# Kernel tuning notes

Measured on AMD Instinct MI355X. Metric: run time of the kernel, lower is better.

The kernel has to match this reference:

```python
import jax, jax.numpy as jnp
import numpy as np

BEFORE_F = 12   # before_block_frames
AFTER_F = 6     # after_block_frames
FD = BEFORE_F // AFTER_F   # frame_duration = 2
K = 49          # cluster_num
L_TOK = 50      # num_tokens = 1 cls + before_cluster_num(49)
WIDTH = 768
B = 64
EPS_LN = 1e-5


def _layer_norm(x, w, b):
    mu = jnp.mean(x, axis=-1, keepdims=True)
    var = jnp.mean((x - mu) ** 2, axis=-1, keepdims=True)
    return (x - mu) / jnp.sqrt(var + EPS_LN) * w + b


def _cdist(a, b):
    # a: [N, L, D], b: [N, K, D] -> euclidean distances [N, L, K]
    d2 = (jnp.sum(a * a, -1)[:, :, None] + jnp.sum(b * b, -1)[:, None, :]
          - 2.0 * jnp.einsum('nld,nkd->nlk', a, b))
    return jnp.sqrt(jnp.maximum(d2, 0.0))


def setup_inputs() -> dict:
    key = jax.random.key(0)
    ks = jax.random.split(key, 4)
    d_in = FD * (L_TOK - 1)   # 98
    d_h = 4 * d_in            # 392
    d_mid = FD * K            # 98
    std = 0.01
    return {
        "x": jax.random.normal(ks[0], (L_TOK, B * BEFORE_F, WIDTH), jnp.float32),
        "fc1_w": jax.random.normal(ks[1], (d_in, d_h), jnp.float32) * std,
        "fc1_b": jnp.zeros((d_h,), jnp.float32),
        "ln1_w": jnp.ones((d_h,), jnp.float32),
        "ln1_b": jnp.zeros((d_h,), jnp.float32),
        "fc2_w": jax.random.normal(ks[2], (d_h, d_mid), jnp.float32) * std,
        "fc2_b": jnp.zeros((d_mid,), jnp.float32),
        "ln2_w": jnp.ones((d_mid,), jnp.float32),
        "ln2_b": jnp.zeros((d_mid,), jnp.float32),
        "fc3_w": jax.random.normal(ks[3], (d_mid, K), jnp.float32) * std,
        "fc3_b": jnp.zeros((K,), jnp.float32),
        "ln3_w": jnp.ones((K,), jnp.float32),
        "ln3_b": jnp.zeros((K,), jnp.float32),
    }


def reference(x, fc1_w, fc1_b, ln1_w, ln1_b, fc2_w, fc2_b, ln2_w, ln2_b,
              fc3_w, fc3_b, ln3_w, ln3_b):
    num_tokens, Bt, width = x.shape
    Bsz = Bt // BEFORE_F
    N = Bsz * AFTER_F
    xt = jnp.transpose(x, (1, 0, 2))                        # [Bt, L, D]

    # class token: mean over each frame_duration group -> [B*after, 1, D]
    cls = xt[:, 0, :].reshape(Bsz, AFTER_F, FD, width).mean(axis=2)
    class_embed = cls.reshape(N, 1, width)

    # patch tokens; torch.cat of splits along dim 0 gives (after, B) ordering
    res = xt[:, 1:, :].reshape(Bsz, AFTER_F, FD, num_tokens - 1, width)
    data = jnp.transpose(res, (1, 0, 2, 3, 4)).reshape(N, FD * (num_tokens - 1), width)
    d_data = jax.lax.stop_gradient(data)

    # token MLP over the token axis: [N, D, FD*(L-1)] -> [N, D, K]
    z = jnp.transpose(d_data, (0, 2, 1))
    z = _layer_norm(z @ fc1_w + fc1_b, ln1_w, ln1_b)
    z = _layer_norm(z @ fc2_w + fc2_b, ln2_w, ln2_b)
    z = _layer_norm(z @ fc3_w + fc3_b, ln3_w, ln3_b)
    centroids = jnp.transpose(z, (0, 2, 1))                 # [N, K, D]

    # wcss cluster loss (training path)
    dm = _cdist(d_data, centroids)                          # [N, L', K]
    cluster_loss = jnp.sum(jnp.min(dm, axis=-1), axis=-1).mean()

    # medoid selection: shift so every distance is negative, then masked min
    dm_s = dm - jnp.max(dm) - 1.0
    cd = jnp.min(dm_s, axis=-1)                             # [N, L']
    assign = jnp.argmin(dm_s, axis=-1)                      # [N, L']
    mask = assign[:, None, :] == jnp.arange(K)[None, :, None]   # [N, K, L']
    vals = jnp.where(mask, cd[:, None, :], 0.0)
    medoids = jnp.sort(jnp.argmin(vals, axis=-1), axis=1)   # [N, K]

    new_data = jnp.take_along_axis(data, medoids[:, :, None], axis=1)  # [N, K, D]
    # reorder (after, B) -> (B, after)
    sampled = jnp.transpose(new_data.reshape(AFTER_F, Bsz, K, width),
                            (1, 0, 2, 3)).reshape(N, K, width)
    out = jnp.concatenate([class_embed, sampled], axis=1)   # [N, K+1, D]
    out = jnp.transpose(out, (1, 0, 2))                     # [K+1, B*after, D]
    return out, cluster_loss
```

## Files before the change

### kernel.cpp

```cpp
#include <hip/hip_runtime.h>
#include <cstddef>

#define WIDTH 768
#define NTOK 98
#define DH 392
#define KCL 49
#define NGRP 384

typedef unsigned short ushort_t;
typedef unsigned int uint_t;
typedef __attribute__((ext_vector_type(4))) float f32x4;
typedef __attribute__((ext_vector_type(8))) short bf16x8;

static __device__ __forceinline__ ushort_t f2bf(float f) {
    union { float f; uint_t u; } v; v.f = f;
    uint_t u = v.u;
    uint_t r = (u + 0x7FFFu + ((u >> 16) & 1u)) >> 16;
    return (ushort_t)r;
}
static __device__ __forceinline__ uint_t pack2(float a, float b) {
    return (uint_t)f2bf(a) | ((uint_t)f2bf(b) << 16);
}

__global__ __launch_bounds__(256) void k_prep(
    const float* __restrict__ w1, const float* __restrict__ b1,
    const float* __restrict__ g1, const float* __restrict__ be1,
    const float* __restrict__ w2, const float* __restrict__ b2,
    const float* __restrict__ g2, const float* __restrict__ be2,
    const float* __restrict__ w3, const float* __restrict__ b3,
    ushort_t* __restrict__ w1T, ushort_t* __restrict__ w2T,
    ushort_t* __restrict__ w3T, float* __restrict__ bias2t)
{
    __shared__ float sb3[64];
    const int tid = threadIdx.x;
    if (blockIdx.x == 0) {
        if (tid < 98) {
            float s = b2[tid];
            for (int j = 0; j < DH; j++) s += be1[j] * w2[j * NTOK + tid];
            bias2t[tid] = s;
        }
        if (tid >= 128 && tid < 177) {
            int c = tid - 128;
            float s = b3[c];
            for (int j = 0; j < NTOK; j++) s += be2[j] * w3[j * KCL + c];
            sb3[c] = s;
        }
    }
    __syncthreads();
    if (blockIdx.x == 0 && tid < 64)
        w3T[tid * 128 + 98] = (tid < KCL) ? f2bf(sb3[tid]) : 0;

    for (int i = blockIdx.x * 256 + tid; i < 400 * 128; i += 1024) {
        int j = i >> 7, k = i & 127;
        float v = 0.f;
        if (j < DH) {
            if (k < NTOK) v = w1[k * DH + j];
            else if (k == NTOK) v = b1[j];
        }
        w1T[i] = f2bf(v);
    }
    for (int i = blockIdx.x * 256 + tid; i < 112 * 416; i += 1024) {
        int o = i / 416, k = i - o * 416;
        float v = 0.f;
        if (o < NTOK && k < DH) v = g1[k] * w2[k * NTOK + o];
        w2T[i] = f2bf(v);
    }
    for (int i = blockIdx.x * 256 + tid; i < 64 * 128; i += 1024) {
        int c = i >> 7, k = i & 127;
        if (k == NTOK) continue;
        float v = 0.f;
        if (c < KCL && k < NTOK) v = g2[k] * w3[k * KCL + c];
        w3T[i] = f2bf(v);
    }
}

__global__ __launch_bounds__(256, 2) void k_mlp(
    const float* __restrict__ x,
    const ushort_t* __restrict__ w1T, const ushort_t* __restrict__ w2T,
    const ushort_t* __restrict__ w3T, const float* __restrict__ bias2t,
    const float* __restrict__ g3, const float* __restrict__ be3,
    float* __restrict__ cent)
{
    __shared__ alignas(16) char smem[50176];

    const int tid = threadIdx.x;
    const int wv = tid >> 6;
    const int l = tid & 63;
    const int g = l >> 4;
    const int c16 = l & 15;

    const int n = blockIdx.x / 12;
    const int d0 = (blockIdx.x % 12) * 64;
    const int a = n >> 6, b = n & 63;
    const int bt0 = b * 12 + a * 2;

    {
        const int m = tid & 63;
        for (int oct = (tid >> 6); oct < 13; oct += 4) {
            ushort_t vals[8];
            #pragma unroll
            for (int e = 0; e < 8; e++) {
                int t = oct * 8 + e;
                float v;
                if (t < NTOK) {
                    int f = (t >= KCL), lt = t - f * KCL;
                    v = x[((size_t)(1 + lt) * WIDTH + bt0 + f) * WIDTH + d0 + m];
                } else v = (t == NTOK) ? 1.0f : 0.0f;
                vals[e] = f2bf(v);
            }
            uint4 u;
            u.x = (uint_t)vals[0] | ((uint_t)vals[1] << 16);
            u.y = (uint_t)vals[2] | ((uint_t)vals[3] << 16);
            u.z = (uint_t)vals[4] | ((uint_t)vals[5] << 16);
            u.w = (uint_t)vals[6] | ((uint_t)vals[7] << 16);
            *(uint4*)(smem + m * 256 + ((oct * 16) ^ ((m & 15) << 4))) = u;
        }
    }
    __syncthreads();

    bf16x8 bv[4];
    {
        const int mrow = wv * 16 + c16;
        #pragma unroll
        for (int ks = 0; ks < 4; ks++) {
            int oct = ks * 4 + g; if (oct > 12) oct = 12;
            bv[ks] = *(const bf16x8*)(smem + mrow * 256 + ((oct * 16) ^ ((mrow & 15) << 4)));
        }
    }
    __syncthreads();

    char* hbase = smem + wv * 12544 + c16 * 784;
    char* h2row = smem + wv * 12544 + c16 * 256;

    f32x4 acc1[25];
    #pragma unroll
    for (int T = 0; T < 25; T++) acc1[T] = (f32x4){0.f, 0.f, 0.f, 0.f};
    #pragma unroll
    for (int ks = 0; ks < 4; ks++) {
        #pragma unroll
        for (int T = 0; T < 25; T++) {
            const bf16x8 av = *(const bf16x8*)(w1T + (T * 16 + c16) * 128 + (ks * 4 + g) * 8);
            acc1[T] = __builtin_amdgcn_mfma_f32_16x16x32_bf16(av, bv[ks], acc1[T], 0, 0, 0);
        }
    }

    {
        float S = 0.f, Q = 0.f;
        #pragma unroll
        for (int T = 0; T < 25; T++) {
            f32x4 v = acc1[T];
            S += v.x + v.y + v.z + v.w;
            Q += v.x * v.x + v.y * v.y + v.z * v.z + v.w * v.w;
        }
        S += __shfl_xor(S, 16); Q += __shfl_xor(Q, 16);
        S += __shfl_xor(S, 32); Q += __shfl_xor(Q, 32);
        float mu = S * (1.f / DH);
        float var = Q * (1.f / DH) - mu * mu;
        float rstd = rsqrtf(fmaxf(var, 0.f) + 1e-5f);
        #pragma unroll
        for (int T = 0; T < 25; T++) {
            if (T == 24 && g >= 2) continue;
            f32x4 v = acc1[T];
            uint2 u;
            u.x = pack2((v.x - mu) * rstd, (v.y - mu) * rstd);
            u.y = pack2((v.z - mu) * rstd, (v.w - mu) * rstd);
            *(uint2*)(hbase + (T * 16 + g * 4) * 2) = u;
        }
    }

    f32x4 acc2[7];
    #pragma unroll
    for (int T = 0; T < 7; T++) acc2[T] = (f32x4){0.f, 0.f, 0.f, 0.f};
    #pragma unroll
    for (int ks = 0; ks < 13; ks++) {
        int oct = ks * 4 + g; if (oct > 48) oct = 48;
        const bf16x8 bvv = *(const bf16x8*)(hbase + oct * 16);
        #pragma unroll
        for (int T = 0; T < 7; T++) {
            const bf16x8 av = *(const bf16x8*)(w2T + (T * 16 + c16) * 416 + (ks * 4 + g) * 8);
            acc2[T] = __builtin_amdgcn_mfma_f32_16x16x32_bf16(av, bvv, acc2[T], 0, 0, 0);
        }
    }

    {
        #pragma unroll
        for (int T = 0; T < 7; T++) {
            int o0 = T * 16 + g * 4;
            #pragma unroll
            for (int r = 0; r < 4; r++) {
                int o = o0 + r;
                if (o < NTOK) acc2[T][r] += bias2t[o];
            }
        }
        float S = 0.f, Q = 0.f;
        #pragma unroll
        for (int T = 0; T < 7; T++) {
            f32x4 v = acc2[T];
            S += v.x + v.y + v.z + v.w;
            Q += v.x * v.x + v.y * v.y + v.z * v.z + v.w * v.w;
        }
        S += __shfl_xor(S, 16); Q += __shfl_xor(Q, 16);
        S += __shfl_xor(S, 32); Q += __shfl_xor(Q, 32);
        float mu = S * (1.f / NTOK);
        float var = Q * (1.f / NTOK) - mu * mu;
        float rstd = rsqrtf(fmaxf(var, 0.f) + 1e-5f);
        const int swz = (c16 & 7) << 4;
        #pragma unroll
        for (int T = 0; T < 7; T++) {
            f32x4 v = acc2[T];
            uint2 u;
            if (T < 6) {
                u.x = pack2((v.x - mu) * rstd, (v.y - mu) * rstd);
                u.y = pack2((v.z - mu) * rstd, (v.w - mu) * rstd);
            } else if (g == 0) {
                u.x = pack2((v.x - mu) * rstd, (v.y - mu) * rstd);
                u.y = pack2(1.0f, 0.0f);
            } else {
                u.x = 0u; u.y = 0u;
            }
            *(uint2*)(h2row + (((T * 16 + g * 4) * 2) ^ swz)) = u;
        }
        uint2 z; z.x = 0u; z.y = 0u;
        *(uint2*)(h2row + (((112 + g * 4) * 2) ^ swz)) = z;
    }

    f32x4 acc3[4];
    #pragma unroll
    for (int T = 0; T < 4; T++) acc3[T] = (f32x4){0.f, 0.f, 0.f, 0.f};
    {
        const int swz = (c16 & 7) << 4;
        #pragma unroll
        for (int ks = 0; ks < 4; ks++) {
            int oct = ks * 4 + g;
            const bf16x8 bvv = *(const bf16x8*)(h2row + ((oct * 16) ^ swz));
            #pragma unroll
            for (int T = 0; T < 4; T++) {
                const bf16x8 av = *(const bf16x8*)(w3T + (T * 16 + c16) * 128 + (ks * 4 + g) * 8);
                acc3[T] = __builtin_amdgcn_mfma_f32_16x16x32_bf16(av, bvv, acc3[T], 0, 0, 0);
            }
        }
    }

    {
        float S = 0.f, Q = 0.f;
        #pragma unroll
        for (int T = 0; T < 4; T++) {
            f32x4 v = acc3[T];
            S += v.x + v.y + v.z + v.w;
            Q += v.x * v.x + v.y * v.y + v.z * v.z + v.w * v.w;
        }
        S += __shfl_xor(S, 16); Q += __shfl_xor(Q, 16);
        S += __shfl_xor(S, 32); Q += __shfl_xor(Q, 32);
        float mu = S * (1.f / KCL);
        float var = Q * (1.f / KCL) - mu * mu;
        float rstd = rsqrtf(fmaxf(var, 0.f) + 1e-5f);
        const size_t cbase = (size_t)n * KCL * WIDTH + d0 + wv * 16 + c16;
        #pragma unroll
        for (int T = 0; T < 4; T++) {
            int c0 = T * 16 + g * 4;
            #pragma unroll
            for (int r = 0; r < 4; r++) {
                int c = c0 + r;
                if (c < KCL) {
                    float val = (acc3[T][r] - mu) * rstd * g3[c] + be3[c];
                    cent[cbase + (size_t)c * WIDTH] = val;
                }
            }
        }
    }
}

__global__ __launch_bounds__(256) void k_dist(
    const float* __restrict__ x, const float* __restrict__ cent,
    float* __restrict__ mind, int* __restrict__ assignp)
{
    int wid = blockIdx.x * 4 + (threadIdx.x >> 6);
    int lane = threadIdx.x & 63;
    int n = wid / 25, g = wid - n * 25;
    int t0 = g * 4;
    int a = n >> 6, b = n & 63;
    int bt0 = b * 12 + a * 2;

    float d[4][12];
    #pragma unroll
    for (int tt = 0; tt < 4; tt++) {
        int t = t0 + tt;
        bool valid = t < NTOK;
        int te = valid ? t : 0;
        int f = te / KCL, l = te - f * KCL;
        const float* src = x + ((size_t)(1 + l) * WIDTH + bt0 + f) * WIDTH + lane;
        #pragma unroll
        for (int i = 0; i < 12; i++) d[tt][i] = valid ? src[i * 64] : 0.f;
    }
    float nd[4];
    #pragma unroll
    for (int tt = 0; tt < 4; tt++) {
        float s = 0.f;
        #pragma unroll
        for (int i = 0; i < 12; i++) s = fmaf(d[tt][i], d[tt][i], s);
        #pragma unroll
        for (int o = 32; o > 0; o >>= 1) s += __shfl_xor(s, o);
        nd[tt] = s;
    }

    float minv[4] = {1e30f, 1e30f, 1e30f, 1e30f};
    int mini[4] = {0, 0, 0, 0};
    for (int k = 0; k < KCL; k++) {
        const float* cr = cent + ((size_t)n * KCL + k) * WIDTH + lane;
        float c[12];
        #pragma unroll
        for (int i = 0; i < 12; i++) c[i] = cr[i * 64];
        float cn = 0.f;
        #pragma unroll
        for (int i = 0; i < 12; i++) cn = fmaf(c[i], c[i], cn);
        float dot[4] = {0.f, 0.f, 0.f, 0.f};
        #pragma unroll
        for (int tt = 0; tt < 4; tt++)
            #pragma unroll
            for (int i = 0; i < 12; i++) dot[tt] = fmaf(d[tt][i], c[i], dot[tt]);
        #pragma unroll
        for (int o = 32; o > 0; o >>= 1) {
            cn += __shfl_xor(cn, o);
            #pragma unroll
            for (int tt = 0; tt < 4; tt++) dot[tt] += __shfl_xor(dot[tt], o);
        }
        #pragma unroll
        for (int tt = 0; tt < 4; tt++) {
            float dist = sqrtf(fmaxf(nd[tt] + cn - 2.f * dot[tt], 0.f));
            if (dist < minv[tt]) { minv[tt] = dist; mini[tt] = k; }
        }
    }
    if (lane == 0) {
        int nt = NTOK - t0; if (nt > 4) nt = 4;
        for (int tt = 0; tt < nt; tt++) {
            mind[n * NTOK + t0 + tt] = minv[tt];
            assignp[n * NTOK + t0 + tt] = mini[tt];
        }
    }
}

__global__ __launch_bounds__(256) void k_medoid(
    const float* __restrict__ x, const float* __restrict__ mind,
    const int* __restrict__ assignp, float* __restrict__ out)
{
    __shared__ float smind[NTOK];
    __shared__ int sassign[NTOK];
    __shared__ int med[KCL], sorted[KCL];

    int n = blockIdx.x, tid = threadIdx.x;
    int a = n >> 6, b = n & 63;
    int np = b * 6 + a;
    int bt0 = b * 12 + a * 2;

    if (tid < NTOK) { smind[tid] = mind[n * NTOK + tid]; sassign[tid] = assignp[n * NTOK + tid]; }
    __syncthreads();

    if (tid < KCL) {
        float best = 1e30f; int bi = 0;
        for (int t = 0; t < NTOK; t++)
            if (sassign[t] == tid && smind[t] < best) { best = smind[t]; bi = t; }
        med[tid] = bi;
    }
    __syncthreads();
    if (tid < KCL) {
        int mk = med[tid], rank = 0;
        for (int j = 0; j < KCL; j++) {
            int mj = med[j];
            rank += (mj < mk) || (mj == mk && j < tid);
        }
        sorted[rank] = mk;
    }
    __syncthreads();

    for (int dd = tid; dd < WIDTH; dd += 256)
        out[(size_t)np * WIDTH + dd] =
            0.5f * (x[(size_t)bt0 * WIDTH + dd] + x[(size_t)(bt0 + 1) * WIDTH + dd]);

    for (int k = 0; k < KCL; k++) {
        int m = sorted[k];
        int f = m / KCL, l = m - f * KCL;
        const float* src = x + ((size_t)(1 + l) * WIDTH + bt0 + f) * WIDTH;
        float* dst = out + ((size_t)(1 + k) * NGRP + np) * WIDTH;
        for (int dd = tid; dd < WIDTH; dd += 256) dst[dd] = src[dd];
    }
}

__global__ __launch_bounds__(256) void k_loss(const float* __restrict__ mind,
                                              float* __restrict__ out_loss)
{
    __shared__ float red[256];
    float s = 0.f;
    for (int i = threadIdx.x; i < NGRP * NTOK; i += 256) s += mind[i];
    red[threadIdx.x] = s;
    __syncthreads();
    for (int o = 128; o > 0; o >>= 1) {
        if (threadIdx.x < o) red[threadIdx.x] += red[threadIdx.x + o];
        __syncthreads();
    }
    if (threadIdx.x == 0) out_loss[0] = red[0] * (1.f / NGRP);
}

extern "C" void kernel_launch(void* const* d_in, const int* in_sizes, int n_in,
                              void* d_out, int out_size, void* d_ws, size_t ws_size,
                              hipStream_t stream)
{
    const float* x   = (const float*)d_in[0];
    const float* w1  = (const float*)d_in[1];
    const float* b1  = (const float*)d_in[2];
    const float* g1  = (const float*)d_in[3];
    const float* be1 = (const float*)d_in[4];
    const float* w2  = (const float*)d_in[5];
    const float* b2  = (const float*)d_in[6];
    const float* g2  = (const float*)d_in[7];
    const float* be2 = (const float*)d_in[8];
    const float* w3  = (const float*)d_in[9];
    const float* b3  = (const float*)d_in[10];
    const float* g3  = (const float*)d_in[11];
    const float* be3 = (const float*)d_in[12];
    float* out = (float*)d_out;

    float* cent = (float*)d_ws;
    float* mind = cent + (size_t)NGRP * KCL * WIDTH;
    int* assignp = (int*)(mind + NGRP * NTOK);
    ushort_t* w1T = (ushort_t*)(assignp + NGRP * NTOK);
    ushort_t* w2T = w1T + 400 * 128;
    ushort_t* w3T = w2T + 112 * 416;
    float* bias2t = (float*)(w3T + 64 * 128);

    k_prep<<<4, 256, 0, stream>>>(w1, b1, g1, be1, w2, b2, g2, be2, w3, b3,
                                  w1T, w2T, w3T, bias2t);
    k_mlp<<<NGRP * 12, 256, 0, stream>>>(x, w1T, w2T, w3T, bias2t, g3, be3, cent);
    k_dist<<<(NGRP * 25) / 4, 256, 0, stream>>>(x, cent, mind, assignp);
    k_medoid<<<NGRP, 256, 0, stream>>>(x, mind, assignp, out);
    k_loss<<<1, 256, 0, stream>>>(mind, out + (out_size - 1));
}
```

Baseline: 859.8 us.

## Defer LayerNorm normalization past next GEMM via rowsum correction, cut register pressure

The first and second LayerNorms are no longer applied before the following GEMM. Raw activations are stored and multiplied, and the normalization is folded in afterwards as rstd*(acc - mu*rowsum(W)) + bias, using row sums and biases precomputed in k_prep. The layer-1 GEMM now runs in chunks of five tiles instead of holding 25 accumulators at once, and the launch bound rises to 3 waves per SIMD to allow higher occupancy. The cost is extra numerical error, because unnormalized values are rounded to bf16 and a mean term is subtracted after accumulation.

```diff
diff --git a/kernel.cpp b/kernel.cpp
--- a/kernel.cpp
+++ b/kernel.cpp
@@ -29,26 +29,41 @@
     const float* __restrict__ g2, const float* __restrict__ be2,
     const float* __restrict__ w3, const float* __restrict__ b3,
     ushort_t* __restrict__ w1T, ushort_t* __restrict__ w2T,
-    ushort_t* __restrict__ w3T, float* __restrict__ bias2t)
-{
-    __shared__ float sb3[64];
+    ushort_t* __restrict__ w3T, float* __restrict__ bias2t,
+    float* __restrict__ rowsum2, float* __restrict__ rowsum3,
+    float* __restrict__ bias3t)
+{
     const int tid = threadIdx.x;
     if (blockIdx.x == 0) {
-        if (tid < 98) {
-            float s = b2[tid];
-            for (int j = 0; j < DH; j++) s += be1[j] * w2[j * NTOK + tid];
-            bias2t[tid] = s;
-        }
-        if (tid >= 128 && tid < 177) {
+        if (tid < 112) {
+            int o = tid;
+            float sb = 0.f, sr = 0.f;
+            if (o < NTOK) {
+                for (int j = 0; j < DH; j++) {
+                    float w = w2[j * NTOK + o];
+                    sb += be1[j] * w;
+                    sr += g1[j] * w;
+                }
+                sb += b2[o];
+            }
+            bias2t[o] = sb;
+            rowsum2[o] = sr;
+        }
+        if (tid >= 128 && tid < 192) {
             int c = tid - 128;
-            float s = b3[c];
-            for (int j = 0; j < NTOK; j++) s += be2[j] * w3[j * KCL + c];
-            sb3[c] = s;
-        }
-    }
-    __syncthreads();
-    if (blockIdx.x == 0 && tid < 64)
-        w3T[tid * 128 + 98] = (tid < KCL) ? f2bf(sb3[tid]) : 0;
+            float sb = 0.f, sr = 0.f;
+            if (c < KCL) {
+                for (int j = 0; j < NTOK; j++) {
+                    float w = w3[j * KCL + c];
+                    sb += be2[j] * w;
+                    sr += g2[j] * w;
+                }
+                sb += b3[c];
+            }
+            bias3t[c] = sb;
+            rowsum3[c] = sr;
+        }
+    }
 
     for (int i = blockIdx.x * 256 + tid; i < 400 * 128; i += 1024) {
         int j = i >> 7, k = i & 127;
@@ -67,17 +82,18 @@
     }
     for (int i = blockIdx.x * 256 + tid; i < 64 * 128; i += 1024) {
         int c = i >> 7, k = i & 127;
-        if (k == NTOK) continue;
         float v = 0.f;
         if (c < KCL && k < NTOK) v = g2[k] * w3[k * KCL + c];
         w3T[i] = f2bf(v);
     }
 }
 
-__global__ __launch_bounds__(256, 2) void k_mlp(
+__global__ __launch_bounds__(256, 3) void k_mlp(
     const float* __restrict__ x,
     const ushort_t* __restrict__ w1T, const ushort_t* __restrict__ w2T,
     const ushort_t* __restrict__ w3T, const float* __restrict__ bias2t,
+    const float* __restrict__ rowsum2, const float* __restrict__ rowsum3,
+    const float* __restrict__ bias3t,
     const float* __restrict__ g3, const float* __restrict__ be3,
     float* __restrict__ cent)
 {
@@ -132,41 +148,38 @@
     char* hbase = smem + wv * 12544 + c16 * 784;
     char* h2row = smem + wv * 12544 + c16 * 256;
 
-    f32x4 acc1[25];
-    #pragma unroll
-    for (int T = 0; T < 25; T++) acc1[T] = (f32x4){0.f, 0.f, 0.f, 0.f};
-    #pragma unroll
-    for (int ks = 0; ks < 4; ks++) {
-        #pragma unroll
-        for (int T = 0; T < 25; T++) {
-            const bf16x8 av = *(const bf16x8*)(w1T + (T * 16 + c16) * 128 + (ks * 4 + g) * 8);
-            acc1[T] = __builtin_amdgcn_mfma_f32_16x16x32_bf16(av, bv[ks], acc1[T], 0, 0, 0);
-        }
-    }
-
-    {
-        float S = 0.f, Q = 0.f;
-        #pragma unroll
-        for (int T = 0; T < 25; T++) {
-            f32x4 v = acc1[T];
-            S += v.x + v.y + v.z + v.w;
-            Q += v.x * v.x + v.y * v.y + v.z * v.z + v.w * v.w;
-        }
-        S += __shfl_xor(S, 16); Q += __shfl_xor(Q, 16);
-        S += __shfl_xor(S, 32); Q += __shfl_xor(Q, 32);
-        float mu = S * (1.f / DH);
-        float var = Q * (1.f / DH) - mu * mu;
-        float rstd = rsqrtf(fmaxf(var, 0.f) + 1e-5f);
-        #pragma unroll
-        for (int T = 0; T < 25; T++) {
-            if (T == 24 && g >= 2) continue;
-            f32x4 v = acc1[T];
-            uint2 u;
-            u.x = pack2((v.x - mu) * rstd, (v.y - mu) * rstd);
-            u.y = pack2((v.z - mu) * rstd, (v.w - mu) * rstd);
-            *(uint2*)(hbase + (T * 16 + g * 4) * 2) = u;
-        }
-    }
+    float S1 = 0.f, Q1 = 0.f;
+    #pragma unroll
+    for (int tc = 0; tc < 25; tc += 5) {
+        f32x4 acc[5];
+        #pragma unroll
+        for (int u = 0; u < 5; u++) acc[u] = (f32x4){0.f, 0.f, 0.f, 0.f};
+        #pragma unroll
+        for (int ks = 0; ks < 4; ks++) {
+            #pragma unroll
+            for (int u = 0; u < 5; u++) {
+                const bf16x8 av = *(const bf16x8*)(w1T + ((tc + u) * 16 + c16) * 128 + (ks * 4 + g) * 8);
+                acc[u] = __builtin_amdgcn_mfma_f32_16x16x32_bf16(av, bv[ks], acc[u], 0, 0, 0);
+            }
+        }
+        #pragma unroll
+        for (int u = 0; u < 5; u++) {
+            int T = tc + u;
+            f32x4 v = acc[u];
+            S1 += v.x + v.y + v.z + v.w;
+            Q1 += v.x * v.x + v.y * v.y + v.z * v.z + v.w * v.w;
+            if (!(T == 24 && g >= 2)) {
+                uint2 uu;
+                uu.x = pack2(v.x, v.y);
+                uu.y = pack2(v.z, v.w);
+                *(uint2*)(hbase + (T * 16 + g * 4) * 2) = uu;
+            }
+        }
+    }
+    S1 += __shfl_xor(S1, 16); Q1 += __shfl_xor(Q1, 16);
+    S1 += __shfl_xor(S1, 32); Q1 += __shfl_xor(Q1, 32);
+    const float mu1 = S1 * (1.f / DH);
+    const float rstd1 = rsqrtf(fmaxf(Q1 * (1.f / DH) - mu1 * mu1, 0.f) + 1e-5f);
 
     f32x4 acc2[7];
     #pragma unroll
@@ -181,44 +194,34 @@
             acc2[T] = __builtin_amdgcn_mfma_f32_16x16x32_bf16(av, bvv, acc2[T], 0, 0, 0);
         }
     }
-
+    float S2 = 0.f, Q2 = 0.f;
+    #pragma unroll
+    for (int T = 0; T < 7; T++) {
+        const int o0 = T * 16 + g * 4;
+        const float4 bs = *(const float4*)(bias2t + o0);
+        const float4 rs = *(const float4*)(rowsum2 + o0);
+        f32x4 v = acc2[T];
+        v.x = rstd1 * (v.x - mu1 * rs.x) + bs.x;
+        v.y = rstd1 * (v.y - mu1 * rs.y) + bs.y;
+        v.z = rstd1 * (v.z - mu1 * rs.z) + bs.z;
+        v.w = rstd1 * (v.w - mu1 * rs.w) + bs.w;
+        acc2[T] = v;
+        S2 += v.x + v.y + v.z + v.w;
+        Q2 += v.x * v.x + v.y * v.y + v.z * v.z + v.w * v.w;
+    }
+    S2 += __shfl_xor(S2, 16); Q2 += __shfl_xor(Q2, 16);
+    S2 += __shfl_xor(S2, 32); Q2 += __shfl_xor(Q2, 32);
+    const float mu2 = S2 * (1.f / NTOK);
+    const float rstd2 = rsqrtf(fmaxf(Q2 * (1.f / NTOK) - mu2 * mu2, 0.f) + 1e-5f);
     {
-        #pragma unroll
-        for (int T = 0; T < 7; T++) {
-            int o0 = T * 16 + g * 4;
-            #pragma unroll
-            for (int r = 0; r < 4; r++) {
-                int o = o0 + r;
-                if (o < NTOK) acc2[T][r] += bias2t[o];
-            }
-        }
-        float S = 0.f, Q = 0.f;
+        const int swz = (c16 & 7) << 4;
         #pragma unroll
         for (int T = 0; T < 7; T++) {
             f32x4 v = acc2[T];
-            S += v.x + v.y + v.z + v.w;
-            Q += v.x * v.x + v.y * v.y + v.z * v.z + v.w * v.w;
-        }
-        S += __shfl_xor(S, 16); Q += __shfl_xor(Q, 16);
-        S += __shfl_xor(S, 32); Q += __shfl_xor(Q, 32);
-        float mu = S * (1.f / NTOK);
-        float var = Q * (1.f / NTOK) - mu * mu;
-        float rstd = rsqrtf(fmaxf(var, 0.f) + 1e-5f);
-        const int swz = (c16 & 7) << 4;
-        #pragma unroll
-        for (int T = 0; T < 7; T++) {
-            f32x4 v = acc2[T];
-            uint2 u;
-            if (T < 6) {
-                u.x = pack2((v.x - mu) * rstd, (v.y - mu) * rstd);
-                u.y = pack2((v.z - mu) * rstd, (v.w - mu) * rstd);
-            } else if (g == 0) {
-                u.x = pack2((v.x - mu) * rstd, (v.y - mu) * rstd);
-                u.y = pack2(1.0f, 0.0f);
-            } else {
-                u.x = 0u; u.y = 0u;
-            }
-            *(uint2*)(h2row + (((T * 16 + g * 4) * 2) ^ swz)) = u;
+            uint2 uu;
+            uu.x = pack2(v.x, v.y);
+            uu.y = pack2(v.z, v.w);
+            *(uint2*)(h2row + (((T * 16 + g * 4) * 2) ^ swz)) = uu;
         }
         uint2 z; z.x = 0u; z.y = 0u;
         *(uint2*)(h2row + (((112 + g * 4) * 2) ^ swz)) = z;
@@ -231,38 +234,44 @@
         const int swz = (c16 & 7) << 4;
         #pragma unroll
         for (int ks = 0; ks < 4; ks++) {
-            int oct = ks * 4 + g;
+            const int oct = ks * 4 + g;
             const bf16x8 bvv = *(const bf16x8*)(h2row + ((oct * 16) ^ swz));
             #pragma unroll
             for (int T = 0; T < 4; T++) {
-                const bf16x8 av = *(const bf16x8*)(w3T + (T * 16 + c16) * 128 + (ks * 4 + g) * 8);
+                const bf16x8 av = *(const bf16x8*)(w3T + (T * 16 + c16) * 128 + oct * 8);
                 acc3[T] = __builtin_amdgcn_mfma_f32_16x16x32_bf16(av, bvv, acc3[T], 0, 0, 0);
             }
         }
     }
-
+    float S3 = 0.f, Q3 = 0.f;
+    #pragma unroll
+    for (int T = 0; T < 4; T++) {
+        const int c0 = T * 16 + g * 4;
+        const float4 bs = *(const float4*)(bias3t + c0);
+        const float4 rs = *(const float4*)(rowsum3 + c0);
+        f32x4 v = acc3[T];
+        v.x = rstd2 * (v.x - mu2 * rs.x) + bs.x;
+        v.y = rstd2 * (v.y - mu2 * rs.y) + bs.y;
+        v.z = rstd2 * (v.z - mu2 * rs.z) + bs.z;
+        v.w = rstd2 * (v.w - mu2 * rs.w) + bs.w;
+        acc3[T] = v;
+        S3 += v.x + v.y + v.z + v.w;
+        Q3 += v.x * v.x + v.y * v.y + v.z * v.z + v.w * v.w;
+    }
+    S3 += __shfl_xor(S3, 16); Q3 += __shfl_xor(Q3, 16);
+    S3 += __shfl_xor(S3, 32); Q3 += __shfl_xor(Q3, 32);
+    const float mu3 = S3 * (1.f / KCL);
+    const float rstd3 = rsqrtf(fmaxf(Q3 * (1.f / KCL) - mu3 * mu3, 0.f) + 1e-5f);
     {
-        float S = 0.f, Q = 0.f;
+        const size_t cbase = (size_t)n * KCL * WIDTH + d0 + wv * 16 + c16;
         #pragma unroll
         for (int T = 0; T < 4; T++) {
-            f32x4 v = acc3[T];
-            S += v.x + v.y + v.z + v.w;
-            Q += v.x * v.x + v.y * v.y + v.z * v.z + v.w * v.w;
-        }
-        S += __shfl_xor(S, 16); Q += __shfl_xor(Q, 16);
-        S += __shfl_xor(S, 32); Q += __shfl_xor(Q, 32);
-        float mu = S * (1.f / KCL);
-        float var = Q * (1.f / KCL) - mu * mu;
-        float rstd = rsqrtf(fmaxf(var, 0.f) + 1e-5f);
-        const size_t cbase = (size_t)n * KCL * WIDTH + d0 + wv * 16 + c16;
-        #pragma unroll
-        for (int T = 0; T < 4; T++) {
-            int c0 = T * 16 + g * 4;
+            const int c0 = T * 16 + g * 4;
             #pragma unroll
             for (int r = 0; r < 4; r++) {
-                int c = c0 + r;
+                const int c = c0 + r;
                 if (c < KCL) {
-                    float val = (acc3[T][r] - mu) * rstd * g3[c] + be3[c];
+                    float val = (acc3[T][r] - mu3) * rstd3 * g3[c] + be3[c];
                     cent[cbase + (size_t)c * WIDTH] = val;
                 }
             }
@@ -426,10 +435,14 @@
     ushort_t* w2T = w1T + 400 * 128;
     ushort_t* w3T = w2T + 112 * 416;
     float* bias2t = (float*)(w3T + 64 * 128);
+    float* rowsum2 = bias2t + 112;
+    float* rowsum3 = rowsum2 + 112;
+    float* bias3t = rowsum3 + 64;
 
     k_prep<<<4, 256, 0, stream>>>(w1, b1, g1, be1, w2, b2, g2, be2, w3, b3,
-                                  w1T, w2T, w3T, bias2t);
-    k_mlp<<<NGRP * 12, 256, 0, stream>>>(x, w1T, w2T, w3T, bias2t, g3, be3, cent);
+                                  w1T, w2T, w3T, bias2t, rowsum2, rowsum3, bias3t);
+    k_mlp<<<NGRP * 12, 256, 0, stream>>>(x, w1T, w2T, w3T, bias2t, rowsum2, rowsum3,
+                                         bias3t, g3, be3, cent);
     k_dist<<<(NGRP * 25) / 4, 256, 0, stream>>>(x, cent, mind, assignp);
     k_medoid<<<NGRP, 256, 0, stream>>>(x, mind, assignp, out);
     k_loss<<<1, 256, 0, stream>>>(mind, out + (out_size - 1));
```

Result: slower. 918.2 us (+6.8%).
